# Performance work log

Hardware: AMD Instinct MI355X
Metric: run time of the kernel (lower is better)

## Reference

```python
import jax, jax.numpy as jnp
import numpy as np

N_NODES = 100000
N_EDGES = 1600000
N_FEAT = 128
HIDDEN = 128
N_CLASSES = 64


def setup_inputs() -> dict:
    key = jax.random.key(0)
    ks = jax.random.split(key, 6)
    x = jax.random.normal(ks[0], (N_NODES, N_FEAT), dtype=jnp.float32)
    edge_index = jax.random.randint(ks[1], (2, N_EDGES), 0, N_NODES, dtype=jnp.int64)
    # Glorot-ish scaled weights
    W1_l = jax.random.normal(ks[2], (N_FEAT, HIDDEN), dtype=jnp.float32) / np.sqrt(N_FEAT)
    W1_r = jax.random.normal(ks[3], (N_FEAT, HIDDEN), dtype=jnp.float32) / np.sqrt(N_FEAT)
    W2_l = jax.random.normal(ks[4], (HIDDEN, N_CLASSES), dtype=jnp.float32) / np.sqrt(HIDDEN)
    W2_r = jax.random.normal(ks[5], (HIDDEN, N_CLASSES), dtype=jnp.float32) / np.sqrt(HIDDEN)
    b1 = jnp.zeros((HIDDEN,), dtype=jnp.float32)
    b2 = jnp.zeros((N_CLASSES,), dtype=jnp.float32)
    return {"x": x, "edge_index": edge_index, "W1_l": W1_l, "b1": b1,
            "W1_r": W1_r, "W2_l": W2_l, "b2": b2, "W2_r": W2_r}


def _sage_conv(h, src, dst, n_nodes, inv_deg, W_l, W_r, b):
    # mean aggregation of source-node features into destination nodes
    agg = jax.ops.segment_sum(h[src], dst, num_segments=n_nodes)  # [N, d]
    agg = agg * inv_deg[:, None]
    return agg @ W_l + h @ W_r + b


def reference(x, edge_index, W1_l, b1, W1_r, W2_l, b2, W2_r):
    src, dst = edge_index[0], edge_index[1]
    n = x.shape[0]
    deg = jax.ops.segment_sum(jnp.ones_like(dst, dtype=x.dtype), dst, num_segments=n)
    inv_deg = 1.0 / jnp.maximum(deg, 1.0)
    h = jax.nn.relu(_sage_conv(x, src, dst, n, inv_deg, W1_l, W1_r, b1))
    # dropout is identity in eval mode
    out = _sage_conv(h, src, dst, n, inv_deg, W2_l, W2_r, b2)
    return out
```

## Files before the change

kernel.cpp:

```cpp
#include <hip/hip_runtime.h>

#define N_NODES   100000
#define N_EDGES   1600000
#define BSHIFT    9
#define NB        196
#define BSTRIDE   9216

typedef __attribute__((ext_vector_type(8))) short short8;
typedef __attribute__((ext_vector_type(4))) float f32x4;
typedef __attribute__((ext_vector_type(2))) float f32x2;

__device__ __forceinline__ unsigned short f2bf(float f) {
    unsigned u = __float_as_uint(f);
    u += 0x7FFF + ((u >> 16) & 1);
    return (unsigned short)(u >> 16);
}

__device__ __forceinline__ int load_src(const int* e, int is64, int i) {
    return is64 ? e[2 * i] : e[i];
}
__device__ __forceinline__ int load_dst(const int* e, int is64, int i) {
    return is64 ? e[2 * (N_EDGES + i)] : e[N_EDGES + i];
}

__device__ __forceinline__ int block_detect_is64(const int* e, int* s_nz) {
    if (threadIdx.x == 0) *s_nz = 0;
    __syncthreads();
    int v = 0;
    for (int i = threadIdx.x; i < 1024; i += 256) v |= e[2 * i + 1];
    if (v) atomicOr(s_nz, 1);
    __syncthreads();
    return (*s_nz == 0) ? 1 : 0;
}

__global__ __launch_bounds__(256) void phaseA_kernel(
        const int* __restrict__ e, const float* __restrict__ x,
        const float* __restrict__ W1_l, const float* __restrict__ W1_r,
        const float* __restrict__ W2_l, const float* __restrict__ W2_r,
        int* __restrict__ bktcur, int* __restrict__ pairs,
        short* __restrict__ xb, unsigned int* __restrict__ xq,
        short* __restrict__ W1t, short* __restrict__ W2lt, short* __restrict__ W2rt) {
    __shared__ int2 s_pairs[4096];
    __shared__ int s_cnt[256], s_off[256], s_base[256], s_cur[256];
    __shared__ int s_nz;
    const int blk = blockIdx.x;
    if (blk < 391) {
        const int tid = threadIdx.x;
        s_cnt[tid] = 0;
        int is64 = block_detect_is64(e, &s_nz);
        __syncthreads();
        int i0 = blk * 4096;
        int n = min(4096, N_EDGES - i0);
        int ls[16], ld[16];
        #pragma unroll
        for (int t = 0; t < 16; t++) {
            int k = t * 256 + tid;
            if (k < n) {
                ls[t] = load_src(e, is64, i0 + k);
                ld[t] = load_dst(e, is64, i0 + k);
                atomicAdd(&s_cnt[ld[t] >> BSHIFT], 1);
            }
        }
        __syncthreads();
        int lv = s_cnt[tid];
        s_off[tid] = lv;
        __syncthreads();
        for (int off = 1; off < 256; off <<= 1) {
            int t = (tid >= off) ? s_off[tid - off] : 0;
            __syncthreads();
            s_off[tid] += t;
            __syncthreads();
        }
        int excl = s_off[tid] - lv;
        int gb = 0;
        if (tid < NB && lv > 0) gb = atomicAdd(&bktcur[tid], lv);
        s_off[tid] = excl;
        s_base[tid] = tid * BSTRIDE + gb;
        s_cur[tid] = excl;
        __syncthreads();
        #pragma unroll
        for (int t = 0; t < 16; t++) {
            int k = t * 256 + tid;
            if (k < n) {
                int pos = atomicAdd(&s_cur[ld[t] >> BSHIFT], 1);
                s_pairs[pos] = (int2){ls[t], ld[t]};
            }
        }
        __syncthreads();
        for (int j = tid; j < n; j += 256) {
            int2 pr = s_pairs[j];
            int b = pr.y >> BSHIFT;
            pairs[s_base[b] + (j - s_off[b])] = pr.x | ((pr.y & 511) << 17);
        }
    } else if (blk < 12891) {
        int t = (blk - 391) * 256 + threadIdx.x;
        int i = t * 4;
        float4 v = *(const float4*)&x[i];
        short4 o;
        o.x = (short)f2bf(v.x); o.y = (short)f2bf(v.y);
        o.z = (short)f2bf(v.z); o.w = (short)f2bf(v.w);
        *(short4*)&xb[i] = o;
        int w = __builtin_amdgcn_cvt_pk_fp8_f32(v.x, v.y, 0, false);
        w = __builtin_amdgcn_cvt_pk_fp8_f32(v.z, v.w, w, true);
        xq[t] = (unsigned int)w;
    } else {
        int i = (blk - 12891) * 256 + threadIdx.x;
        if (i < 32768) {
            int n = i >> 8, k = i & 255;
            float v = (k < 128) ? W1_l[k * 128 + n] : W1_r[(k - 128) * 128 + n];
            W1t[i] = (short)f2bf(v);
        } else if (i < 40960) {
            int j = i - 32768, n = j >> 7, k = j & 127;
            W2lt[j] = (short)f2bf(W2_l[k * 64 + n]);
        } else {
            int j = i - 40960, n = j >> 7, k = j & 127;
            W2rt[j] = (short)f2bf(W2_r[k * 64 + n]);
        }
    }
}

__global__ __launch_bounds__(512) void fused_fill_kernel(
        const int* __restrict__ bktcur, const int* __restrict__ pairs,
        int* __restrict__ deg_i, int* __restrict__ cursor,
        float* __restrict__ inv_deg, int* __restrict__ col) {
    __shared__ int ldeg[512];
    __shared__ int ssum[512];
    const int tid = threadIdx.x;
    const int b = blockIdx.x;
    const int nbase = b << BSHIFT;
    ldeg[tid] = 0;
    __syncthreads();
    const int cnt = bktcur[b];
    const int p0 = b * BSTRIDE;
    for (int j = tid; j < cnt; j += 512)
        atomicAdd(&ldeg[pairs[p0 + j] >> 17], 1);
    __syncthreads();
    int d = ldeg[tid];
    ssum[tid] = d;
    __syncthreads();
    for (int off = 1; off < 512; off <<= 1) {
        int t = (tid >= off) ? ssum[tid - off] : 0;
        __syncthreads();
        ssum[tid] += t;
        __syncthreads();
    }
    int s = p0 + ssum[tid] - d;
    int node = nbase + tid;
    if (node < N_NODES) {
        deg_i[node] = d;
        cursor[node] = s;
        inv_deg[node] = 1.0f / fmaxf((float)d, 1.0f);
    }
    ldeg[tid] = s;
    __syncthreads();
    for (int j = tid; j < cnt; j += 512) {
        int pk = pairs[p0 + j];
        int pos = atomicAdd(&ldeg[pk >> 17], 1);
        col[pos] = pk & 0x1FFFF;
    }
}

__device__ __forceinline__ void acc_fp8x8(float* acc, uint2 w) {
    f32x2 f;
    f = __builtin_amdgcn_cvt_pk_f32_fp8((int)w.x, false); acc[0] += f[0]; acc[1] += f[1];
    f = __builtin_amdgcn_cvt_pk_f32_fp8((int)w.x, true);  acc[2] += f[0]; acc[3] += f[1];
    f = __builtin_amdgcn_cvt_pk_f32_fp8((int)w.y, false); acc[4] += f[0]; acc[5] += f[1];
    f = __builtin_amdgcn_cvt_pk_f32_fp8((int)w.y, true);  acc[6] += f[0]; acc[7] += f[1];
}

__global__ __launch_bounds__(256) void agg128_kernel(
        const int* __restrict__ cursor, const int* __restrict__ deg_i,
        const int* __restrict__ col, const unsigned int* __restrict__ xq,
        const float* __restrict__ inv_deg, short* __restrict__ agg) {
    int node = blockIdx.x * 16 + (threadIdx.x >> 4);
    int lane = threadIdx.x & 15;
    int cnt = deg_i[node];
    int start = cursor[node];
    float acc[8] = {0.f};
    int k = 0;
    for (; k + 8 <= cnt; k += 8) {
        int s[8];
        #pragma unroll
        for (int j = 0; j < 8; j++) s[j] = col[start + k + j];
        uint2 w[8];
        #pragma unroll
        for (int j = 0; j < 8; j++)
            w[j] = *(const uint2*)(xq + (size_t)s[j] * 32 + lane * 2);
        #pragma unroll
        for (int j = 0; j < 8; j++) acc_fp8x8(acc, w[j]);
    }
    for (; k < cnt; k++) {
        uint2 w = *(const uint2*)(xq + (size_t)col[start + k] * 32 + lane * 2);
        acc_fp8x8(acc, w);
    }
    float sc = inv_deg[node];
    short8 o;
    #pragma unroll
    for (int j = 0; j < 8; j++) o[j] = (short)f2bf(acc[j] * sc);
    *(short8*)(agg + (size_t)node * 128 + lane * 8) = o;
}

__global__ __launch_bounds__(256) void agg64_kernel(
        const int* __restrict__ cursor, const int* __restrict__ deg_i,
        const int* __restrict__ col, const unsigned int* __restrict__ pq,
        const float* __restrict__ inv_deg, float* __restrict__ out) {
    int node = blockIdx.x * 32 + (threadIdx.x >> 3);
    int lane = threadIdx.x & 7;
    int cnt = deg_i[node];
    int start = cursor[node];
    float sc = inv_deg[node];
    float* dst = out + (size_t)node * 64 + lane * 8;
    float4 r0 = *(float4*)dst;
    float4 r1 = *(float4*)(dst + 4);
    float acc[8] = {0.f};
    int k = 0;
    for (; k + 8 <= cnt; k += 8) {
        int s[8];
        #pragma unroll
        for (int j = 0; j < 8; j++) s[j] = col[start + k + j];
        uint2 w[8];
        #pragma unroll
        for (int j = 0; j < 8; j++)
            w[j] = *(const uint2*)(pq + (size_t)s[j] * 16 + lane * 2);
        #pragma unroll
        for (int j = 0; j < 8; j++) acc_fp8x8(acc, w[j]);
    }
    for (; k < cnt; k++) {
        uint2 w = *(const uint2*)(pq + (size_t)col[start + k] * 16 + lane * 2);
        acc_fp8x8(acc, w);
    }
    r0.x += acc[0] * sc; r0.y += acc[1] * sc; r0.z += acc[2] * sc; r0.w += acc[3] * sc;
    r1.x += acc[4] * sc; r1.y += acc[5] * sc; r1.z += acc[6] * sc; r1.w += acc[7] * sc;
    *(float4*)dst = r0;
    *(float4*)(dst + 4) = r1;
}

__global__ __launch_bounds__(256, 4) void gemm12_mfma(
        const short* __restrict__ agg1, const short* __restrict__ xb,
        const short* __restrict__ W1t, const float* __restrict__ b1,
        const short* __restrict__ W2lt, const short* __restrict__ W2rt,
        const float* __restrict__ b2,
        unsigned char* __restrict__ p8, float* __restrict__ out) {
    __shared__ __align__(16) char hsb[8192];
    const int wave = threadIdx.x >> 6, lane = threadIdx.x & 63;
    const int m = lane & 15, q = lane >> 4;
    const int P = blockIdx.x;

    short8 a[2][8];
    #pragma unroll
    for (int tt = 0; tt < 2; tt++) {
        const short* arow = agg1 + (size_t)((2 * P + tt) * 16 + m) * 128;
        const short* xrow = xb   + (size_t)((2 * P + tt) * 16 + m) * 128;
        #pragma unroll
        for (int c = 0; c < 4; c++) {
            a[tt][c]     = *(const short8*)(arow + c * 32 + q * 8);
            a[tt][c + 4] = *(const short8*)(xrow + c * 32 + q * 8);
        }
    }
    float bias1[2];
    bias1[0] = b1[wave * 32 + m];
    bias1[1] = b1[wave * 32 + 16 + m];

    f32x4 acc1[2][2];
    #pragma unroll
    for (int tt = 0; tt < 2; tt++)
        #pragma unroll
        for (int t = 0; t < 2; t++) acc1[tt][t] = (f32x4){0.f, 0.f, 0.f, 0.f};
    #pragma unroll
    for (int c = 0; c < 8; c++) {
        short8 br0 = *(const short8*)(W1t + (size_t)(wave * 32 + m) * 256 + c * 32 + q * 8);
        short8 br1 = *(const short8*)(W1t + (size_t)(wave * 32 + 16 + m) * 256 + c * 32 + q * 8);
        #pragma unroll
        for (int tt = 0; tt < 2; tt++) {
            acc1[tt][0] = __builtin_amdgcn_mfma_f32_16x16x32_bf16(a[tt][c], br0, acc1[tt][0], 0, 0, 0);
            acc1[tt][1] = __builtin_amdgcn_mfma_f32_16x16x32_bf16(a[tt][c], br1, acc1[tt][1], 0, 0, 0);
        }
    }
    const int wb = wave * 64 + m * 2;
    #pragma unroll
    for (int tt = 0; tt < 2; tt++)
        #pragma unroll
        for (int t = 0; t < 2; t++)
            #pragma unroll
            for (int r = 0; r < 4; r++) {
                int row = tt * 16 + q * 4 + r;
                int byteoff = row * 256 + ((wb + t * 32) ^ ((row & 7) << 4));
                float v = fmaxf(acc1[tt][t][r] + bias1[t], 0.f);
                *(short*)(hsb + byteoff) = (short)f2bf(v);
            }
    __syncthreads();
    const int pw = wave & 1;
    const short* Wp = (wave < 2) ? W2lt : W2rt;
    float bias2[2];
    bias2[0] = b2[pw * 32 + m];
    bias2[1] = b2[pw * 32 + 16 + m];
    const int rsw = (m & 7) << 4;
    f32x4 acc2[2][2];
    #pragma unroll
    for (int tt = 0; tt < 2; tt++) {
        short8 a2[4];
        int rowbyte = (tt * 16 + m) * 256;
        #pragma unroll
        for (int c = 0; c < 4; c++)
            a2[c] = *(const short8*)(hsb + rowbyte + ((q * 16 + c * 64) ^ rsw));
        #pragma unroll
        for (int t = 0; t < 2; t++) acc2[tt][t] = (f32x4){0.f, 0.f, 0.f, 0.f};
        #pragma unroll
        for (int c = 0; c < 4; c++) {
            short8 w20 = *(const short8*)(Wp + (size_t)(pw * 32 + m) * 128 + c * 32 + q * 8);
            short8 w21 = *(const short8*)(Wp + (size_t)(pw * 32 + 16 + m) * 128 + c * 32 + q * 8);
            acc2[tt][0] = __builtin_amdgcn_mfma_f32_16x16x32_bf16(a2[c], w20, acc2[tt][0], 0, 0, 0);
            acc2[tt][1] = __builtin_amdgcn_mfma_f32_16x16x32_bf16(a2[c], w21, acc2[tt][1], 0, 0, 0);
        }
    }
    if (wave < 2) {
        #pragma unroll
        for (int tt = 0; tt < 2; tt++)
            #pragma unroll
            for (int t = 0; t < 2; t++) {
                int colc = pw * 32 + t * 16 + m;
                #pragma unroll
                for (int r = 0; r < 4; r++) {
                    int rr = (2 * P + tt) * 16 + q * 4 + r;
                    float pv = acc2[tt][t][r];
                    int w8 = __builtin_amdgcn_cvt_pk_fp8_f32(pv, pv, 0, false);
                    p8[(size_t)rr * 64 + colc] = (unsigned char)(w8 & 0xFF);
                }
            }
    } else {
        #pragma unroll
        for (int tt = 0; tt < 2; tt++)
            #pragma unroll
            for (int t = 0; t < 2; t++) {
                int colc = pw * 32 + t * 16 + m;
                #pragma unroll
                for (int r = 0; r < 4; r++) {
                    int rr = (2 * P + tt) * 16 + q * 4 + r;
                    out[(size_t)rr * 64 + colc] = acc2[tt][t][r] + bias2[t];
                }
            }
    }
}

extern "C" void kernel_launch(void* const* d_in, const int* in_sizes, int n_in,
                              void* d_out, int out_size, void* d_ws, size_t ws_size,
                              hipStream_t stream) {
    const float* x    = (const float*)d_in[0];
    const int*   edge = (const int*)d_in[1];
    const float* W1_l = (const float*)d_in[2];
    const float* b1   = (const float*)d_in[3];
    const float* W1_r = (const float*)d_in[4];
    const float* W2_l = (const float*)d_in[5];
    const float* b2   = (const float*)d_in[6];
    const float* W2_r = (const float*)d_in[7];
    float* out = (float*)d_out;

    int* iw = (int*)d_ws;
    int* deg_i  = iw;
    int* cursor = iw + 100000;
    int* bktcur = iw + 200000;
    float* inv_deg = (float*)(iw + 200256);
    int* col    = iw + 300352;
    short* xb   = (short*)(iw + 2106688);
    short* hb   = xb + 12800000;
    short* ag1  = hb + 12800000;
    short* W1t  = ag1 + 12800000;
    short* W2lt = W1t + 32768;
    short* W2rt = W2lt + 8192;
    unsigned int* xq = (unsigned int*)hb;
    int* pairs = (int*)ag1;
    unsigned char* p8 = (unsigned char*)hb;
    unsigned int*  pq = (unsigned int*)hb;

    hipMemsetAsync(bktcur, 0, 256 * sizeof(int), stream);

    phaseA_kernel<<<13083, 256, 0, stream>>>(edge, x, W1_l, W1_r, W2_l, W2_r,
                                             bktcur, pairs, xb, xq, W1t, W2lt, W2rt);
    fused_fill_kernel<<<NB, 512, 0, stream>>>(bktcur, pairs, deg_i, cursor, inv_deg, col);

    agg128_kernel<<<6250, 256, 0, stream>>>(cursor, deg_i, col, xq, inv_deg, ag1);
    gemm12_mfma<<<3125, 256, 0, stream>>>(ag1, xb, W1t, b1, W2lt, W2rt, b2, p8, out);
    agg64_kernel<<<3125, 256, 0, stream>>>(cursor, deg_i, col, pq, inv_deg, out);
}
```

Before: 268.9 us.

## Make fused GEMM kernel persistent with register-resident weights and next-tile prefetch

The fused two-layer GEMM kernel becomes a persistent grid of 1024 blocks that loop over row tiles with a stride of 1024. Weight fragments and biases are loaded into registers once per block, and the next tile's activations are prefetched while the current tile's MFMAs run. A double-buffered LDS hidden tile lets one barrier per iteration suffice. The aim is to cut repeated weight loads and hide global load latency, at the cost of more registers and lower occupancy (launch bounds drop from 4 to 2 waves per SIMD).

```diff
diff --git a/kernel.cpp b/kernel.cpp
--- a/kernel.cpp
+++ b/kernel.cpp
@@ -235,17 +235,40 @@
     *(float4*)(dst + 4) = r1;
 }
 
-__global__ __launch_bounds__(256, 4) void gemm12_mfma(
+__global__ __launch_bounds__(256, 2) void gemm12_mfma(
         const short* __restrict__ agg1, const short* __restrict__ xb,
         const short* __restrict__ W1t, const float* __restrict__ b1,
         const short* __restrict__ W2lt, const short* __restrict__ W2rt,
         const float* __restrict__ b2,
         unsigned char* __restrict__ p8, float* __restrict__ out) {
-    __shared__ __align__(16) char hsb[8192];
+    __shared__ __align__(16) char hs[2][8192];
     const int wave = threadIdx.x >> 6, lane = threadIdx.x & 63;
     const int m = lane & 15, q = lane >> 4;
-    const int P = blockIdx.x;
-
+
+    short8 breg[2][8];
+    #pragma unroll
+    for (int t = 0; t < 2; t++)
+        #pragma unroll
+        for (int c = 0; c < 8; c++)
+            breg[t][c] = *(const short8*)(W1t + (size_t)(wave * 32 + t * 16 + m) * 256 + c * 32 + q * 8);
+    float bias1[2];
+    bias1[0] = b1[wave * 32 + m];
+    bias1[1] = b1[wave * 32 + 16 + m];
+
+    const int pw = wave & 1;
+    const short* Wp = (wave < 2) ? W2lt : W2rt;
+    short8 w2[2][4];
+    #pragma unroll
+    for (int t = 0; t < 2; t++)
+        #pragma unroll
+        for (int c = 0; c < 4; c++)
+            w2[t][c] = *(const short8*)(Wp + (size_t)(pw * 32 + t * 16 + m) * 128 + c * 32 + q * 8);
+    float bias2[2];
+    bias2[0] = b2[pw * 32 + m];
+    bias2[1] = b2[pw * 32 + 16 + m];
+
+    int P = blockIdx.x;
+    if (P >= 3125) return;
     short8 a[2][8];
     #pragma unroll
     for (int tt = 0; tt < 2; tt++) {
@@ -257,88 +280,94 @@
             a[tt][c + 4] = *(const short8*)(xrow + c * 32 + q * 8);
         }
     }
-    float bias1[2];
-    bias1[0] = b1[wave * 32 + m];
-    bias1[1] = b1[wave * 32 + 16 + m];
-
-    f32x4 acc1[2][2];
-    #pragma unroll
-    for (int tt = 0; tt < 2; tt++)
-        #pragma unroll
-        for (int t = 0; t < 2; t++) acc1[tt][t] = (f32x4){0.f, 0.f, 0.f, 0.f};
-    #pragma unroll
-    for (int c = 0; c < 8; c++) {
-        short8 br0 = *(const short8*)(W1t + (size_t)(wave * 32 + m) * 256 + c * 32 + q * 8);
-        short8 br1 = *(const short8*)(W1t + (size_t)(wave * 32 + 16 + m) * 256 + c * 32 + q * 8);
-        #pragma unroll
-        for (int tt = 0; tt < 2; tt++) {
-            acc1[tt][0] = __builtin_amdgcn_mfma_f32_16x16x32_bf16(a[tt][c], br0, acc1[tt][0], 0, 0, 0);
-            acc1[tt][1] = __builtin_amdgcn_mfma_f32_16x16x32_bf16(a[tt][c], br1, acc1[tt][1], 0, 0, 0);
-        }
-    }
     const int wb = wave * 64 + m * 2;
-    #pragma unroll
-    for (int tt = 0; tt < 2; tt++)
-        #pragma unroll
-        for (int t = 0; t < 2; t++)
-            #pragma unroll
-            for (int r = 0; r < 4; r++) {
-                int row = tt * 16 + q * 4 + r;
-                int byteoff = row * 256 + ((wb + t * 32) ^ ((row & 7) << 4));
-                float v = fmaxf(acc1[tt][t][r] + bias1[t], 0.f);
-                *(short*)(hsb + byteoff) = (short)f2bf(v);
-            }
-    __syncthreads();
-    const int pw = wave & 1;
-    const short* Wp = (wave < 2) ? W2lt : W2rt;
-    float bias2[2];
-    bias2[0] = b2[pw * 32 + m];
-    bias2[1] = b2[pw * 32 + 16 + m];
     const int rsw = (m & 7) << 4;
-    f32x4 acc2[2][2];
-    #pragma unroll
-    for (int tt = 0; tt < 2; tt++) {
-        short8 a2[4];
-        int rowbyte = (tt * 16 + m) * 256;
-        #pragma unroll
-        for (int c = 0; c < 4; c++)
-            a2[c] = *(const short8*)(hsb + rowbyte + ((q * 16 + c * 64) ^ rsw));
-        #pragma unroll
-        for (int t = 0; t < 2; t++) acc2[tt][t] = (f32x4){0.f, 0.f, 0.f, 0.f};
-        #pragma unroll
-        for (int c = 0; c < 4; c++) {
-            short8 w20 = *(const short8*)(Wp + (size_t)(pw * 32 + m) * 128 + c * 32 + q * 8);
-            short8 w21 = *(const short8*)(Wp + (size_t)(pw * 32 + 16 + m) * 128 + c * 32 + q * 8);
-            acc2[tt][0] = __builtin_amdgcn_mfma_f32_16x16x32_bf16(a2[c], w20, acc2[tt][0], 0, 0, 0);
-            acc2[tt][1] = __builtin_amdgcn_mfma_f32_16x16x32_bf16(a2[c], w21, acc2[tt][1], 0, 0, 0);
-        }
-    }
-    if (wave < 2) {
+    int buf = 0;
+    while (true) {
+        f32x4 acc[2][2];
         #pragma unroll
         for (int tt = 0; tt < 2; tt++)
             #pragma unroll
-            for (int t = 0; t < 2; t++) {
-                int colc = pw * 32 + t * 16 + m;
-                #pragma unroll
-                for (int r = 0; r < 4; r++) {
-                    int rr = (2 * P + tt) * 16 + q * 4 + r;
-                    float pv = acc2[tt][t][r];
-                    int w8 = __builtin_amdgcn_cvt_pk_fp8_f32(pv, pv, 0, false);
-                    p8[(size_t)rr * 64 + colc] = (unsigned char)(w8 & 0xFF);
+            for (int t = 0; t < 2; t++) acc[tt][t] = (f32x4){0.f, 0.f, 0.f, 0.f};
+        #pragma unroll
+        for (int c = 0; c < 8; c++)
+            #pragma unroll
+            for (int tt = 0; tt < 2; tt++)
+                #pragma unroll
+                for (int t = 0; t < 2; t++)
+                    acc[tt][t] = __builtin_amdgcn_mfma_f32_16x16x32_bf16(a[tt][c], breg[t][c], acc[tt][t], 0, 0, 0);
+        int Pn = P + 1024;
+        if (Pn < 3125) {
+            #pragma unroll
+            for (int tt = 0; tt < 2; tt++) {
+                const short* arow = agg1 + (size_t)((2 * Pn + tt) * 16 + m) * 128;
+                const short* xrow = xb   + (size_t)((2 * Pn + tt) * 16 + m) * 128;
+                #pragma unroll
+                for (int c = 0; c < 4; c++) {
+                    a[tt][c]     = *(const short8*)(arow + c * 32 + q * 8);
+                    a[tt][c + 4] = *(const short8*)(xrow + c * 32 + q * 8);
                 }
             }
-    } else {
+        }
+        char* hb0 = hs[buf];
         #pragma unroll
         for (int tt = 0; tt < 2; tt++)
             #pragma unroll
-            for (int t = 0; t < 2; t++) {
-                int colc = pw * 32 + t * 16 + m;
+            for (int t = 0; t < 2; t++)
                 #pragma unroll
                 for (int r = 0; r < 4; r++) {
-                    int rr = (2 * P + tt) * 16 + q * 4 + r;
-                    out[(size_t)rr * 64 + colc] = acc2[tt][t][r] + bias2[t];
+                    int row = tt * 16 + q * 4 + r;
+                    int byteoff = row * 256 + ((wb + t * 32) ^ ((row & 7) << 4));
+                    float v = fmaxf(acc[tt][t][r] + bias1[t], 0.f);
+                    *(short*)(hb0 + byteoff) = (short)f2bf(v);
                 }
-            }
+        __syncthreads();
+        f32x4 acc2[2][2];
+        #pragma unroll
+        for (int tt = 0; tt < 2; tt++) {
+            short8 a2[4];
+            int rowbyte = (tt * 16 + m) * 256;
+            #pragma unroll
+            for (int c = 0; c < 4; c++)
+                a2[c] = *(const short8*)(hb0 + rowbyte + ((q * 16 + c * 64) ^ rsw));
+            #pragma unroll
+            for (int t = 0; t < 2; t++) acc2[tt][t] = (f32x4){0.f, 0.f, 0.f, 0.f};
+            #pragma unroll
+            for (int c = 0; c < 4; c++)
+                #pragma unroll
+                for (int t = 0; t < 2; t++)
+                    acc2[tt][t] = __builtin_amdgcn_mfma_f32_16x16x32_bf16(a2[c], w2[t][c], acc2[tt][t], 0, 0, 0);
+        }
+        if (wave < 2) {
+            #pragma unroll
+            for (int tt = 0; tt < 2; tt++)
+                #pragma unroll
+                for (int t = 0; t < 2; t++) {
+                    int colc = pw * 32 + t * 16 + m;
+                    #pragma unroll
+                    for (int r = 0; r < 4; r++) {
+                        int rr = (2 * P + tt) * 16 + q * 4 + r;
+                        float pv = acc2[tt][t][r];
+                        int w8 = __builtin_amdgcn_cvt_pk_fp8_f32(pv, pv, 0, false);
+                        p8[(size_t)rr * 64 + colc] = (unsigned char)(w8 & 0xFF);
+                    }
+                }
+        } else {
+            #pragma unroll
+            for (int tt = 0; tt < 2; tt++)
+                #pragma unroll
+                for (int t = 0; t < 2; t++) {
+                    int colc = pw * 32 + t * 16 + m;
+                    #pragma unroll
+                    for (int r = 0; r < 4; r++) {
+                        int rr = (2 * P + tt) * 16 + q * 4 + r;
+                        out[(size_t)rr * 64 + colc] = acc2[tt][t][r] + bias2[t];
+                    }
+                }
+        }
+        if (Pn >= 3125) break;
+        P = Pn;
+        buf ^= 1;
     }
 }
 
@@ -379,6 +408,6 @@
     fused_fill_kernel<<<NB, 512, 0, stream>>>(bktcur, pairs, deg_i, cursor, inv_deg, col);
 
     agg128_kernel<<<6250, 256, 0, stream>>>(cursor, deg_i, col, xq, inv_deg, ag1);
-    gemm12_mfma<<<3125, 256, 0, stream>>>(ag1, xb, W1t, b1, W2lt, W2rt, b2, p8, out);
+    gemm12_mfma<<<1024, 256, 0, stream>>>(ag1, xb, W1t, b1, W2lt, W2rt, b2, p8, out);
     agg64_kernel<<<3125, 256, 0, stream>>>(cursor, deg_i, col, pq, inv_deg, out);
 }
```

Result: faster. 248.3 us (-7.7%).
